# Kernel tuning notes

Hardware: AMD Instinct MI355X
Metric: run time of the kernel (lower is better)

Reference implementation:

```python
import jax, jax.numpy as jnp
import numpy as np

D_IN = 1024
D_OUT = 1024
NUM_HEADS = 16
HEAD_DIM = D_OUT // NUM_HEADS


def setup_inputs() -> dict:
    key = jax.random.key(0)
    ks = jax.random.split(key, 6)
    s = 0.02
    return {
        "x": jax.random.normal(ks[0], (4, 2048, D_IN), dtype=jnp.float32),
        "Wq": jax.random.normal(ks[1], (D_IN, D_OUT), dtype=jnp.float32) * s,
        "Wk": jax.random.normal(ks[2], (D_IN, D_OUT), dtype=jnp.float32) * s,
        "Wv": jax.random.normal(ks[3], (D_IN, D_OUT), dtype=jnp.float32) * s,
        "Wo": jax.random.normal(ks[4], (D_OUT, D_OUT), dtype=jnp.float32) * s,
        "bo": jax.random.normal(ks[5], (D_OUT,), dtype=jnp.float32) * s,
    }


def reference(x, Wq, Wk, Wv, Wo, bo):
    B, S, _ = x.shape
    # QKV projections (no bias), split into heads: [B, H, S, Dh]
    def split_heads(t):
        return t.reshape(B, S, NUM_HEADS, HEAD_DIM).transpose(0, 2, 1, 3)

    q = split_heads(x @ Wq)
    k = split_heads(x @ Wk)
    v = split_heads(x @ Wv)

    # causal scores [B, H, S, S]; note: original masks BEFORE scaling,
    # but -inf is scale-invariant so softmax(scores/sqrt(d)) with mask is identical.
    scores = jnp.einsum("bhqd,bhkd->bhqk", q, k) / jnp.sqrt(jnp.asarray(HEAD_DIM, x.dtype))
    causal = jnp.tril(jnp.ones((S, S), dtype=bool))
    scores = jnp.where(causal, scores, -jnp.inf)
    attn = jax.nn.softmax(scores, axis=-1)
    # dropout p=0.0 -> identity
    ctx = jnp.einsum("bhqk,bhkd->bhqd", attn, v)  # [B, H, S, Dh]
    ctx = ctx.transpose(0, 2, 1, 3).reshape(B, S, D_OUT)
    return ctx @ Wo + bo
```

## Files before the change

kernel.cpp:

```cpp
#include <hip/hip_runtime.h>
#include <hip/hip_bf16.h>
#include <math.h>


typedef __attribute__((ext_vector_type(8))) short short8;
typedef __attribute__((ext_vector_type(4))) float f32x4;

#define MFMA_BF16(a, b, c) __builtin_amdgcn_mfma_f32_16x16x32_bf16((a), (b), (c), 0, 0, 0)

#define SBAR() asm volatile("s_barrier" ::: "memory")
#define VMCNT6() asm volatile("s_waitcnt vmcnt(6)" ::: "memory")
#define VMCNT0() asm volatile("s_waitcnt vmcnt(0)" ::: "memory")

__device__ __forceinline__ void gld_lds16(const void* g, void* l) {
  __builtin_amdgcn_global_load_lds((const __attribute__((address_space(1))) void*)g,
                                   (__attribute__((address_space(3))) void*)l, 16, 0, 0);
}

__global__ void prep_kernel(const float* __restrict__ x, __hip_bfloat16* __restrict__ xb,
                            const float* __restrict__ W0, const float* __restrict__ W1,
                            const float* __restrict__ W2, const float* __restrict__ W3,
                            __hip_bfloat16* __restrict__ T0, __hip_bfloat16* __restrict__ T1,
                            __hip_bfloat16* __restrict__ T2, __hip_bfloat16* __restrict__ T3) {
  const int bid = blockIdx.x, tid = threadIdx.x;
  if (bid < 8192) {
    int i = bid * 256 + tid;
    float4 v = ((const float4*)x)[i];
    __align__(8) __hip_bfloat16 tmp[4] = {__float2bfloat16(v.x), __float2bfloat16(v.y),
                                          __float2bfloat16(v.z), __float2bfloat16(v.w)};
    ((ushort4*)xb)[i] = *(const ushort4*)tmp;
  } else {
    int zz = bid - 8192;
    int z = zz >> 10, rem = zz & 1023;
    const float* W = (z == 0) ? W0 : (z == 1) ? W1 : (z == 2) ? W2 : W3;
    __hip_bfloat16* Wt = (z == 0) ? T0 : (z == 1) ? T1 : (z == 2) ? T2 : T3;
    __shared__ float tile[32][33];
    int tx = tid & 31, ty = tid >> 5;
    int n0 = (rem & 31) * 32, k0 = (rem >> 5) * 32;
#pragma unroll
    for (int i = 0; i < 4; ++i)
      tile[ty + i * 8][tx] = W[(size_t)(k0 + ty + i * 8) * 1024 + n0 + tx];
    __syncthreads();
#pragma unroll
    for (int i = 0; i < 4; ++i)
      Wt[(size_t)(n0 + ty + i * 8) * 1024 + k0 + tx] = __float2bfloat16(tile[tx][ty + i * 8]);
  }
}

__device__ __forceinline__ void gemm8p_kloop(
    const __hip_bfloat16* __restrict__ A, const __hip_bfloat16* __restrict__ Bt,
    int m0, int gn0, __hip_bfloat16* As_, __hip_bfloat16* Bs_,
    f32x4 (&acc)[4][4]) {
  const int tid = threadIdx.x;
  const int lane = tid & 63, wid = tid >> 6;
  const int quad = lane >> 4, l16 = lane & 15;
  const int wm = (wid >> 1) * 64, wn = (wid & 1) * 64;
  const int sw = l16 & 7;

  auto stage_half = [&](int t, int half, int slot) {
#pragma unroll
    for (int li = 0; li < 2; ++li) {
      int sbase = __builtin_amdgcn_readfirstlane((half * 2 + li) * 512 + wid * 64);
      int s = sbase + lane, row = s >> 3, ch = (s & 7) ^ (row & 7);
      gld_lds16(A + (size_t)(m0 + row) * 1024 + t * 64 + ch * 8,
                As_ + slot * 16384 + sbase * 8);
    }
    {
      int sbase = __builtin_amdgcn_readfirstlane(half * 512 + wid * 64);
      int s = sbase + lane, row = s >> 3, ch = (s & 7) ^ (row & 7);
      gld_lds16(Bt + (size_t)(gn0 + row) * 1024 + t * 64 + ch * 8,
                Bs_ + slot * 8192 + sbase * 8);
    }
  };

  auto tile_step = [&](int t, int cur, int st, int mode) {
    const __hip_bfloat16* Asl = As_ + cur * 16384;
    const __hip_bfloat16* Bsl = Bs_ + cur * 8192;
    short8 af[4][2], bf01[2][2], bf23[2][2];
#pragma unroll
    for (int mt = 0; mt < 4; ++mt)
#pragma unroll
      for (int kc = 0; kc < 2; ++kc)
        af[mt][kc] = *(const short8*)&Asl[(wm + mt * 16 + l16) * 64 +
                                          (((kc * 4 + quad) ^ sw) << 3)];
#pragma unroll
    for (int nt = 0; nt < 2; ++nt)
#pragma unroll
      for (int kc = 0; kc < 2; ++kc)
        bf01[nt][kc] = *(const short8*)&Bsl[(wn + nt * 16 + l16) * 64 +
                                            (((kc * 4 + quad) ^ sw) << 3)];
    if (mode == 0) stage_half(t + 2, 0, st);
    if (mode != 2) SBAR();
    __builtin_amdgcn_s_setprio(1);
#pragma unroll
    for (int kc = 0; kc < 2; ++kc)
#pragma unroll
      for (int mt = 0; mt < 4; ++mt)
#pragma unroll
        for (int nt = 0; nt < 2; ++nt)
          acc[mt][nt] = MFMA_BF16(af[mt][kc], bf01[nt][kc], acc[mt][nt]);
    __builtin_amdgcn_s_setprio(0);
    if (mode != 2) SBAR();
#pragma unroll
    for (int nt = 0; nt < 2; ++nt)
#pragma unroll
      for (int kc = 0; kc < 2; ++kc)
        bf23[nt][kc] = *(const short8*)&Bsl[(wn + (2 + nt) * 16 + l16) * 64 +
                                            (((kc * 4 + quad) ^ sw) << 3)];
    if (mode == 0) stage_half(t + 2, 1, st);
    if (mode != 2) SBAR();
    __builtin_amdgcn_s_setprio(1);
#pragma unroll
    for (int kc = 0; kc < 2; ++kc)
#pragma unroll
      for (int mt = 0; mt < 4; ++mt)
#pragma unroll
        for (int nt = 0; nt < 2; ++nt)
          acc[mt][2 + nt] = MFMA_BF16(af[mt][kc], bf23[nt][kc], acc[mt][2 + nt]);
    __builtin_amdgcn_s_setprio(0);
    if (mode == 0) VMCNT6();
    if (mode == 1) VMCNT0();
    if (mode != 2) SBAR();
  };

#pragma unroll
  for (int h = 0; h < 2; ++h) stage_half(0, h, 0);
#pragma unroll
  for (int h = 0; h < 2; ++h) stage_half(1, h, 1);
  VMCNT6();
  SBAR();

  int cur = 0, st = 2;
#pragma unroll 1
  for (int t = 0; t < 14; ++t) {
    tile_step(t, cur, st, 0);
    cur = (cur == 2) ? 0 : cur + 1;
    st = (st == 2) ? 0 : st + 1;
  }
  tile_step(14, 2, 0, 1);
  tile_step(15, 0, 0, 2);
}

__global__ __launch_bounds__(512, 2) void gemm_qkv(
    const __hip_bfloat16* __restrict__ A, const __hip_bfloat16* __restrict__ Bt,
    __hip_bfloat16* __restrict__ q, __hip_bfloat16* __restrict__ k,
    __hip_bfloat16* __restrict__ vT) {
  __shared__ __align__(16) __hip_bfloat16 As[3 * 256 * 64];
  __shared__ __align__(16) __hip_bfloat16 Bs[3 * 128 * 64];
  const int tid = threadIdx.x;
  const int lane = tid & 63, wid = tid >> 6;
  const int quad = lane >> 4, l16 = lane & 15;
  const int part = blockIdx.x >> 3;
  const int n0l = (blockIdx.x & 7) * 128;
  const int gn0 = part * 1024 + n0l;
  const int m0 = blockIdx.y * 256;
  const int wm = (wid >> 1) * 64, wn = (wid & 1) * 64;

  f32x4 acc[4][4] = {};
  gemm8p_kloop(A, Bt, m0, gn0, As, Bs, acc);

  const float CSCL = 0.18033688011112042f;
  if (part < 2) {
    __hip_bfloat16* C = (part == 0) ? q : k;
    const float scl = (part == 0) ? CSCL : 1.0f;
#pragma unroll
    for (int mt = 0; mt < 4; ++mt)
#pragma unroll
      for (int nt = 0; nt < 4; ++nt) {
        int row = m0 + wm + mt * 16 + quad * 4;
        int col = n0l + wn + nt * 16 + l16;
#pragma unroll
        for (int r = 0; r < 4; ++r)
          C[(size_t)(row + r) * 1024 + col] = __float2bfloat16(acc[mt][nt][r] * scl);
      }
  } else {
#pragma unroll
    for (int mt = 0; mt < 4; ++mt)
#pragma unroll
      for (int nt = 0; nt < 4; ++nt) {
        int row = m0 + wm + mt * 16 + quad * 4;
        int nn = n0l + wn + nt * 16 + l16;
        __align__(8) __hip_bfloat16 p4[4];
#pragma unroll
        for (int r = 0; r < 4; ++r) p4[r] = __float2bfloat16(acc[mt][nt][r]);
        *(ushort4*)(vT + (size_t)nn * 8192 + row) = *(const ushort4*)p4;
      }
  }
}

__global__ __launch_bounds__(512, 2) void gemm_bt_f32out(
    const __hip_bfloat16* __restrict__ A, const __hip_bfloat16* __restrict__ Bt,
    float* __restrict__ C, const float* __restrict__ bias) {
  __shared__ __align__(16) __hip_bfloat16 As[3 * 256 * 64];
  __shared__ __align__(16) __hip_bfloat16 Bs[3 * 128 * 64];
  const int tid = threadIdx.x;
  const int lane = tid & 63, wid = tid >> 6;
  const int quad = lane >> 4, l16 = lane & 15;
  const int n0 = blockIdx.x * 128, m0 = blockIdx.y * 256;
  const int wm = (wid >> 1) * 64, wn = (wid & 1) * 64;

  f32x4 acc[4][4] = {};
  gemm8p_kloop(A, Bt, m0, n0, As, Bs, acc);

#pragma unroll
  for (int mt = 0; mt < 4; ++mt)
#pragma unroll
    for (int nt = 0; nt < 4; ++nt) {
      int row = m0 + wm + mt * 16 + quad * 4;
      int col = n0 + wn + nt * 16 + l16;
      float b = bias[col];
#pragma unroll
      for (int r = 0; r < 4; ++r)
        C[(size_t)(row + r) * 1024 + col] = acc[mt][nt][r] + b;
    }
}

__global__ __launch_bounds__(256, 2) void attn_kernel(
    const __hip_bfloat16* __restrict__ Q, const __hip_bfloat16* __restrict__ Km,
    const __hip_bfloat16* __restrict__ vT, __hip_bfloat16* __restrict__ ctx) {
  const int bid = blockIdx.x;
  const int xcd = bid & 7, loc = bid >> 3;
  const int grp = xcd * 8 + (loc >> 3);
  const int p = loc & 7;
  const int h = grp & 15, b = grp >> 4;
  const size_t rbase = (size_t)b * 2048;
  const int tid = threadIdx.x, lane = tid & 63, wid = tid >> 6;
  const int quad = lane >> 4, l16 = lane & 15;
  const int sw = l16 & 7;

  __shared__ __align__(16) __hip_bfloat16 Ks[2][64 * 64];
  __shared__ __align__(16) __hip_bfloat16 Vs[2][64 * 64];
  __shared__ __align__(16) __hip_bfloat16 Ps[4][32 * 64];

  const float NEG_BIG = -1e30f;

#pragma unroll 1
  for (int sub = 0; sub < 2; ++sub) {
    const int t = sub ? (15 - p) : p;
    const int q0 = t * 128;
    const int qw = q0 + wid * 32;
    const int nkt = 2 * t + 2;

    __syncthreads();
    {
#pragma unroll
      for (int i = 0; i < 2; ++i) {
        int sbase = __builtin_amdgcn_readfirstlane(i * 256 + wid * 64);
        int s = sbase + lane, row = s >> 3, lch = (s & 7) ^ (row & 7);
        gld_lds16(Km + (rbase + row) * 1024 + h * 64 + lch * 8, &Ks[0][sbase * 8]);
        gld_lds16(vT + (size_t)(h * 64 + row) * 8192 + rbase + lch * 8, &Vs[0][sbase * 8]);
      }
    }

    short8 qf[2][2];
#pragma unroll
    for (int mt = 0; mt < 2; ++mt)
#pragma unroll
      for (int kc = 0; kc < 2; ++kc)
        qf[mt][kc] = *(const short8*)(Q + (rbase + qw + mt * 16 + l16) * 1024 +
                                      h * 64 + kc * 32 + quad * 8);

    f32x4 o[2][4] = {};
    float lp[2] = {0.f, 0.f};

#pragma unroll 1
    for (int kt = 0; kt < nkt; ++kt) {
      const int cur = kt & 1;
      const int kbase = kt * 64;
      __syncthreads();
      if (kt + 1 < nkt) {
        const int kb = kbase + 64;
#pragma unroll
        for (int i = 0; i < 2; ++i) {
          int sbase = __builtin_amdgcn_readfirstlane(i * 256 + wid * 64);
          int s = sbase + lane, row = s >> 3, lch = (s & 7) ^ (row & 7);
          gld_lds16(Km + (rbase + kb + row) * 1024 + h * 64 + lch * 8,
                    &Ks[cur ^ 1][sbase * 8]);
          gld_lds16(vT + (size_t)(h * 64 + row) * 8192 + rbase + kb + lch * 8,
                    &Vs[cur ^ 1][sbase * 8]);
        }
      }
      const __hip_bfloat16* Kb = &Ks[cur][0];
      const __hip_bfloat16* Vb = &Vs[cur][0];

      if (kbase <= qw + 31) {
        short8 kf[4][2];
#pragma unroll
        for (int nt = 0; nt < 4; ++nt)
#pragma unroll
          for (int kc = 0; kc < 2; ++kc)
            kf[nt][kc] = *(const short8*)&Kb[(nt * 16 + l16) * 64 +
                                             (((kc * 4 + quad) ^ sw) << 3)];
        f32x4 sv[2][4];
#pragma unroll
        for (int mt = 0; mt < 2; ++mt)
#pragma unroll
          for (int nt = 0; nt < 4; ++nt) {
            f32x4 z = {0.f, 0.f, 0.f, 0.f};
            z = MFMA_BF16(kf[nt][0], qf[mt][0], z);
            z = MFMA_BF16(kf[nt][1], qf[mt][1], z);
            sv[mt][nt] = z;
          }
        if (kbase + 63 > qw) {
#pragma unroll
          for (int mt = 0; mt < 2; ++mt)
#pragma unroll
            for (int nt = 0; nt < 4; ++nt)
#pragma unroll
              for (int r = 0; r < 4; ++r) {
                int kpos = kbase + nt * 16 + quad * 4 + r;
                int qrow = qw + mt * 16 + l16;
                if (kpos > qrow) sv[mt][nt][r] = NEG_BIG;
              }
        }
#pragma unroll
        for (int mt = 0; mt < 2; ++mt)
#pragma unroll
          for (int nt = 0; nt < 4; ++nt) {
            __align__(8) __hip_bfloat16 p4[4];
#pragma unroll
            for (int r = 0; r < 4; ++r) {
              float pv = __builtin_amdgcn_exp2f(sv[mt][nt][r]);
              lp[mt] += pv;
              p4[r] = __float2bfloat16(pv);
            }
            int row = mt * 16 + l16;
            int c16 = (nt * 2 + (quad >> 1)) ^ (row & 7);
            *(ushort4*)&Ps[wid][row * 64 + c16 * 8 + (quad & 1) * 4] =
                *(const ushort4*)p4;
          }
        short8 pa[2][2];
#pragma unroll
        for (int mt = 0; mt < 2; ++mt)
#pragma unroll
          for (int kc = 0; kc < 2; ++kc)
            pa[mt][kc] = *(const short8*)&Ps[wid][(mt * 16 + l16) * 64 +
                                                  (((kc * 4 + quad) ^ sw) << 3)];
        short8 vf[4][2];
#pragma unroll
        for (int dt = 0; dt < 4; ++dt)
#pragma unroll
          for (int kc = 0; kc < 2; ++kc)
            vf[dt][kc] = *(const short8*)&Vb[(dt * 16 + l16) * 64 +
                                             (((kc * 4 + quad) ^ sw) << 3)];
#pragma unroll
        for (int mt = 0; mt < 2; ++mt)
#pragma unroll
          for (int dt = 0; dt < 4; ++dt) {
            o[mt][dt] = MFMA_BF16(pa[mt][0], vf[dt][0], o[mt][dt]);
            o[mt][dt] = MFMA_BF16(pa[mt][1], vf[dt][1], o[mt][dt]);
          }
      }
    }

#pragma unroll
    for (int mt = 0; mt < 2; ++mt) {
      lp[mt] += __shfl_xor(lp[mt], 16, 64);
      lp[mt] += __shfl_xor(lp[mt], 32, 64);
    }
#pragma unroll
    for (int mt = 0; mt < 2; ++mt) {
      float inv[4];
#pragma unroll
      for (int r = 0; r < 4; ++r)
        inv[r] = 1.f / __shfl(lp[mt], quad * 4 + r, 64);
#pragma unroll
      for (int dt = 0; dt < 4; ++dt)
#pragma unroll
        for (int r = 0; r < 4; ++r)
          ctx[(rbase + qw + mt * 16 + quad * 4 + r) * 1024 + h * 64 + dt * 16 + l16] =
              __float2bfloat16(o[mt][dt][r] * inv[r]);
    }
  }
}

extern "C" void kernel_launch(void* const* d_in, const int* in_sizes, int n_in,
                              void* d_out, int out_size, void* d_ws, size_t ws_size,
                              hipStream_t stream) {
  const float* x  = (const float*)d_in[0];
  const float* Wq = (const float*)d_in[1];
  const float* Wk = (const float*)d_in[2];
  const float* Wv = (const float*)d_in[3];
  const float* Wo = (const float*)d_in[4];
  const float* bo = (const float*)d_in[5];
  float* out = (float*)d_out;

  char* ws = (char*)d_ws;
  const size_t MB = 1024ull * 1024ull;
  __hip_bfloat16* q   = (__hip_bfloat16*)(ws);
  __hip_bfloat16* k   = (__hip_bfloat16*)(ws + 16 * MB);
  __hip_bfloat16* vT  = (__hip_bfloat16*)(ws + 32 * MB);
  __hip_bfloat16* woT = (__hip_bfloat16*)(ws + 48 * MB);
  __hip_bfloat16* ctx = q;

  char* outc = (char*)d_out;
  __hip_bfloat16* xb    = (__hip_bfloat16*)(outc);
  __hip_bfloat16* wcatT = (__hip_bfloat16*)(outc + 16 * MB);

  prep_kernel<<<8192 + 4096, 256, 0, stream>>>(
      x, xb, Wq, Wk, Wv, Wo,
      wcatT, wcatT + 1024 * 1024, wcatT + 2048 * 1024, woT);

  gemm_qkv<<<dim3(24, 32), 512, 0, stream>>>(xb, wcatT, q, k, vT);

  attn_kernel<<<512, 256, 0, stream>>>(q, k, vT, ctx);

  gemm_bt_f32out<<<dim3(8, 32), 512, 0, stream>>>(ctx, woT, out, bo);
}
```

Baseline: 233.0 us.

## Replace pipelined 256x128 QKV GEMM with simple 128x128 single-buffer tiled kernel

The QKV projection GEMM stops using the triple-buffered 256x128 k-loop shared with the output GEMM. It now uses a standalone kernel with 128x128 tiles, K-chunks of 128, a single LDS buffer, and 256 threads per block, launched on twice as many blocks. This gives more blocks and simpler control flow, but drops the overlap of global loads with MFMA compute because every k-step syncs and loads before computing.

New measurement: 228.2 us. 2.1% less time.

```diff
diff --git a/kernel.cpp b/kernel.cpp
--- a/kernel.cpp
+++ b/kernel.cpp
@@ -47,6 +47,83 @@
   }
 }
 
+__global__ __launch_bounds__(256, 2) void gemm_qkv(
+    const __hip_bfloat16* __restrict__ A, const __hip_bfloat16* __restrict__ Bt,
+    __hip_bfloat16* __restrict__ q, __hip_bfloat16* __restrict__ k,
+    __hip_bfloat16* __restrict__ vT) {
+  __shared__ __align__(16) __hip_bfloat16 As[128 * 128];
+  __shared__ __align__(16) __hip_bfloat16 Bs[128 * 128];
+  const int tid = threadIdx.x;
+  const int lane = tid & 63, wid = tid >> 6;
+  const int quad = lane >> 4, l16 = lane & 15;
+  const int part = blockIdx.x >> 3;
+  const int n0 = (blockIdx.x & 7) * 128;
+  const int gn0 = part * 1024 + n0;
+  const int m0 = blockIdx.y * 128;
+  const int wm = (wid & 1) * 64, wn = (wid >> 1) * 64;
+  const int swz = l16 & 7;
+
+  f32x4 acc[4][4] = {};
+
+  for (int k0 = 0; k0 < 1024; k0 += 128) {
+    __syncthreads();
+#pragma unroll
+    for (int i = 0; i < 8; ++i) {
+      int sbase = __builtin_amdgcn_readfirstlane(wid * 512 + i * 64);
+      int s = sbase + lane;
+      int row = s >> 4;
+      int ch = (s & 15) ^ (row & 7);
+      gld_lds16(A + (size_t)(m0 + row) * 1024 + k0 + ch * 8, &As[sbase * 8]);
+      gld_lds16(Bt + (size_t)(gn0 + row) * 1024 + k0 + ch * 8, &Bs[sbase * 8]);
+    }
+    __syncthreads();
+
+#pragma unroll
+    for (int kc = 0; kc < 4; ++kc) {
+      short8 af[4], bfr[4];
+#pragma unroll
+      for (int t = 0; t < 4; ++t) {
+        int chp = (kc * 4 + quad) ^ swz;
+        af[t]  = *(const short8*)&As[(wm + t * 16 + l16) * 128 + chp * 8];
+        bfr[t] = *(const short8*)&Bs[(wn + t * 16 + l16) * 128 + chp * 8];
+      }
+#pragma unroll
+      for (int mt = 0; mt < 4; ++mt)
+#pragma unroll
+        for (int nt = 0; nt < 4; ++nt)
+          acc[mt][nt] = MFMA_BF16(af[mt], bfr[nt], acc[mt][nt]);
+    }
+  }
+
+  const float CSCL = 0.18033688011112042f;
+  if (part < 2) {
+    __hip_bfloat16* C = (part == 0) ? q : k;
+    const float scl = (part == 0) ? CSCL : 1.0f;
+#pragma unroll
+    for (int mt = 0; mt < 4; ++mt)
+#pragma unroll
+      for (int nt = 0; nt < 4; ++nt) {
+        int row = m0 + wm + mt * 16 + quad * 4;
+        int col = n0 + wn + nt * 16 + l16;
+#pragma unroll
+        for (int r = 0; r < 4; ++r)
+          C[(size_t)(row + r) * 1024 + col] = __float2bfloat16(acc[mt][nt][r] * scl);
+      }
+  } else {
+#pragma unroll
+    for (int mt = 0; mt < 4; ++mt)
+#pragma unroll
+      for (int nt = 0; nt < 4; ++nt) {
+        int row = m0 + wm + mt * 16 + quad * 4;
+        int nn = n0 + wn + nt * 16 + l16;
+        __align__(8) __hip_bfloat16 p4[4];
+#pragma unroll
+        for (int r = 0; r < 4; ++r) p4[r] = __float2bfloat16(acc[mt][nt][r]);
+        *(ushort4*)(vT + (size_t)nn * 8192 + row) = *(const ushort4*)p4;
+      }
+  }
+}
+
 __device__ __forceinline__ void gemm8p_kloop(
     const __hip_bfloat16* __restrict__ A, const __hip_bfloat16* __restrict__ Bt,
     int m0, int gn0, __hip_bfloat16* As_, __hip_bfloat16* Bs_,
@@ -139,53 +216,6 @@
   }
   tile_step(14, 2, 0, 1);
   tile_step(15, 0, 0, 2);
-}
-
-__global__ __launch_bounds__(512, 2) void gemm_qkv(
-    const __hip_bfloat16* __restrict__ A, const __hip_bfloat16* __restrict__ Bt,
-    __hip_bfloat16* __restrict__ q, __hip_bfloat16* __restrict__ k,
-    __hip_bfloat16* __restrict__ vT) {
-  __shared__ __align__(16) __hip_bfloat16 As[3 * 256 * 64];
-  __shared__ __align__(16) __hip_bfloat16 Bs[3 * 128 * 64];
-  const int tid = threadIdx.x;
-  const int lane = tid & 63, wid = tid >> 6;
-  const int quad = lane >> 4, l16 = lane & 15;
-  const int part = blockIdx.x >> 3;
-  const int n0l = (blockIdx.x & 7) * 128;
-  const int gn0 = part * 1024 + n0l;
-  const int m0 = blockIdx.y * 256;
-  const int wm = (wid >> 1) * 64, wn = (wid & 1) * 64;
-
-  f32x4 acc[4][4] = {};
-  gemm8p_kloop(A, Bt, m0, gn0, As, Bs, acc);
-
-  const float CSCL = 0.18033688011112042f;
-  if (part < 2) {
-    __hip_bfloat16* C = (part == 0) ? q : k;
-    const float scl = (part == 0) ? CSCL : 1.0f;
-#pragma unroll
-    for (int mt = 0; mt < 4; ++mt)
-#pragma unroll
-      for (int nt = 0; nt < 4; ++nt) {
-        int row = m0 + wm + mt * 16 + quad * 4;
-        int col = n0l + wn + nt * 16 + l16;
-#pragma unroll
-        for (int r = 0; r < 4; ++r)
-          C[(size_t)(row + r) * 1024 + col] = __float2bfloat16(acc[mt][nt][r] * scl);
-      }
-  } else {
-#pragma unroll
-    for (int mt = 0; mt < 4; ++mt)
-#pragma unroll
-      for (int nt = 0; nt < 4; ++nt) {
-        int row = m0 + wm + mt * 16 + quad * 4;
-        int nn = n0l + wn + nt * 16 + l16;
-        __align__(8) __hip_bfloat16 p4[4];
-#pragma unroll
-        for (int r = 0; r < 4; ++r) p4[r] = __float2bfloat16(acc[mt][nt][r]);
-        *(ushort4*)(vT + (size_t)nn * 8192 + row) = *(const ushort4*)p4;
-      }
-  }
 }
 
 __global__ __launch_bounds__(512, 2) void gemm_bt_f32out(
@@ -401,7 +431,7 @@
       x, xb, Wq, Wk, Wv, Wo,
       wcatT, wcatT + 1024 * 1024, wcatT + 2048 * 1024, woT);
 
-  gemm_qkv<<<dim3(24, 32), 512, 0, stream>>>(xb, wcatT, q, k, vT);
+  gemm_qkv<<<dim3(24, 64), 256, 0, stream>>>(xb, wcatT, q, k, vT);
 
   attn_kernel<<<512, 256, 0, stream>>>(q, k, vT, ctx);
 
```
